# Performance work log

Measured on AMD Instinct MI355X. Metric: run time of the kernel, lower is better.

Reference implementation:

```python
import jax, jax.numpy as jnp
import numpy as np

N_WIRES = 8


def setup_inputs() -> dict:
    key = jax.random.key(0)
    k1, k2, k3 = jax.random.split(key, 3)
    B, S, E = 8, 1024, 64
    x = jax.random.normal(k1, (B, S, E), jnp.float32)
    theta = jax.random.normal(k2, (N_WIRES,), jnp.float32) * 0.1  # trainable RX angles (shared QLayer across heads)
    V_CAT = 16
    combine_w = jax.random.normal(k3, (E, V_CAT), jnp.float32) / jnp.sqrt(jnp.float32(V_CAT))
    combine_b = jnp.zeros((E,), jnp.float32)
    return {"x": x, "theta": theta, "combine_w": combine_w, "combine_b": combine_b}


def _cnot(state, c, t):
    # state: [N] + [2]*N_WIRES ; wire w lives on axis w+1
    ca, ta = c + 1, t + 1
    s0 = jax.lax.index_in_dim(state, 0, axis=ca, keepdims=False)
    s1 = jax.lax.index_in_dim(state, 1, axis=ca, keepdims=False)
    ta2 = ta - 1 if ta > ca else ta  # control axis was removed
    s1 = jnp.flip(s1, axis=ta2)      # flip target bit where control == 1
    return jnp.stack([s0, s1], axis=ca)


def _qlayer(angles, theta):
    # angles: [N, 8]. RX(x) then trainable RX(theta) on same wire == RX(x+theta).
    half = 0.5 * (angles + theta)
    amp0 = jnp.cos(half).astype(jnp.complex64)          # <0|RX|0>
    amp1 = (-1j) * jnp.sin(half).astype(jnp.complex64)  # <1|RX|0>
    N = angles.shape[0]
    # product state over 8 wires -> [N, 256]
    state = jnp.ones((N, 1), jnp.complex64)
    for w in range(N_WIRES):
        per = jnp.stack([amp0[:, w], amp1[:, w]], axis=-1)  # [N, 2]
        state = (state[:, :, None] * per[:, None, :]).reshape(N, -1)
    state = state.reshape((N,) + (2,) * N_WIRES)
    # CNOT chain 0->1, ..., 6->7, then ring closure 7->0
    for w in range(N_WIRES - 1):
        state = _cnot(state, w, w + 1)
    state = _cnot(state, N_WIRES - 1, 0)
    probs = state.real ** 2 + state.imag ** 2
    exps = []
    for w in range(N_WIRES):
        axes = tuple(ax for ax in range(1, N_WIRES + 1) if ax != w + 1)
        marg = probs.sum(axis=axes)  # [N, 2]
        exps.append(marg[:, 0] - marg[:, 1])  # <Z_w>
    return jnp.stack(exps, axis=-1)  # [N, 8]


def reference(x, theta, combine_w, combine_b):
    B, S, E = x.shape
    d_k = E // N_WIRES  # == 8 (encoder needs exactly 8 angles)
    heads = x.reshape(B, S, N_WIRES, d_k).transpose(0, 2, 1, 3)  # [B, H, S, 8]
    meas = _qlayer(heads.reshape(-1, d_k), theta).reshape(B, N_WIRES, S, N_WIRES)
    # torch.chunk(3, -1) on size 8 -> splits of 3, 3, 2
    q, k, v = meas[..., :3], meas[..., 3:6], meas[..., 6:]
    scores = jnp.einsum('bhsd,bhtd->bhst', q, k) / jnp.sqrt(jnp.float32(E))
    attn = jax.nn.softmax(scores, axis=-1)
    out = jnp.einsum('bhst,bhtd->bhsd', attn, v)          # [B, H, S, 2]
    out = out.transpose(0, 2, 1, 3).reshape(B, S, -1)     # [B, S, 16]
    return out @ combine_w.T + combine_b
```

## Files before the change

kernel.cpp:

```cpp
#include <hip/hip_runtime.h>
#include <hip/hip_fp16.h>

#define NB 8
#define NS 1024
#define NH 8

typedef float f2 __attribute__((ext_vector_type(2)));


__global__ __launch_bounds__(256, 2) void attn_fused(
        const float* __restrict__ x, const float* __restrict__ theta,
        float* __restrict__ att) {
    __shared__ float4 kvl[NS];
    __shared__ float  v1l[NS];
    __shared__ float  redS[4][128];
    __shared__ float  redA[4][128];
    __shared__ float  redB[4][128];

    const int tid = threadIdx.x;
    const int bh = blockIdx.x >> 3;
    const int chunk = blockIdx.x & 7;
    const int b = bh >> 3, h = bh & 7;
    const int s0 = chunk * 128;

    float th[8];
#pragma unroll
    for (int j = 0; j < 8; ++j) th[j] = theta[j];

#pragma unroll
    for (int i = 0; i < 4; ++i) {
        int t = tid + i * 256;
        const float4* xp = (const float4*)(x + (((size_t)(b * NS + t)) << 6) + h * 8);
        float4 lo = xp[0], hi = xp[1];
        float c0 = __cosf(lo.x + th[0]);
        float c1 = __cosf(lo.y + th[1]);
        float c2 = __cosf(lo.z + th[2]);
        float c3 = __cosf(lo.w + th[3]);
        float c4 = __cosf(hi.x + th[4]);
        float c5 = __cosf(hi.y + th[5]);
        float c6 = __cosf(hi.z + th[6]);
        float c7 = __cosf(hi.w + th[7]);
        float m3 = ((c0 * c1) * c2) * c3;
        float m4 = m3 * c4;
        float m5 = m4 * c5;
        float m6 = m5 * c6;
        kvl[t] = make_float4(m3, m4, m5, m6);
        v1l[t] = m6 * c7;
    }

    const int ja = tid & 63;
    const int slice = tid >> 6;
    f2 qx, qy, qz;
#pragma unroll
    for (int i = 0; i < 2; ++i) {
        int s = s0 + ja + i * 64;
        const float4* xp = (const float4*)(x + (((size_t)(b * NS + s)) << 6) + h * 8);
        float4 lo = xp[0], hi = xp[1];
        float c0 = __cosf(lo.x + th[0]);
        float c1 = __cosf(lo.y + th[1]);
        float c2 = __cosf(lo.z + th[2]);
        float c3 = __cosf(lo.w + th[3]);
        float c4 = __cosf(hi.x + th[4]);
        float c5 = __cosf(hi.y + th[5]);
        float c6 = __cosf(hi.z + th[6]);
        float c7 = __cosf(hi.w + th[7]);
        float m1 = c0 * c1;
        float m2 = m1 * c2;
        float m0 = ((c1 * c2) * (c3 * c4)) * ((c5 * c6) * c7);
        qx[i] = m0 * 0.125f;
        qy[i] = m1 * 0.125f;
        qz[i] = m2 * 0.125f;
    }
    __syncthreads();

    f2 sum = {0.f, 0.f}, a0 = {0.f, 0.f}, a1 = {0.f, 0.f};
    const int t0 = slice * 256;
#pragma unroll 8
    for (int i = 0; i < 256; ++i) {
        int t = t0 + i;
        float4 kv = kvl[t];
        float v1 = v1l[t];
        f2 d = qx * kv.x + qy * kv.y + qz * kv.z;
        f2 e = {__expf(d.x), __expf(d.y)};
        sum += e;
        a0 += e * kv.w;
        a1 += e * v1;
    }
    redS[slice][ja] = sum.x;  redS[slice][64 + ja] = sum.y;
    redA[slice][ja] = a0.x;   redA[slice][64 + ja] = a0.y;
    redB[slice][ja] = a1.x;   redB[slice][64 + ja] = a1.y;
    __syncthreads();

    if (tid < 128) {
        float S = redS[0][tid] + redS[1][tid] + redS[2][tid] + redS[3][tid];
        float A = redA[0][tid] + redA[1][tid] + redA[2][tid] + redA[3][tid];
        float B = redB[0][tid] + redB[1][tid] + redB[2][tid] + redB[3][tid];
        float inv = 1.0f / S;
        int s = s0 + tid;
        float* o = att + ((size_t)(b * NS + s) * 16) + h * 2;
        o[0] = A * inv;
        o[1] = B * inv;
    }
}

__global__ __launch_bounds__(256, 2) void proj_kernel(
        const float* __restrict__ att, const float* __restrict__ W,
        const float* __restrict__ bias, float* __restrict__ out) {
    __shared__ float WtL[16 * 65];
    __shared__ float biasL[64];
    __shared__ float rowsL[16 * 16];
    const int tid = threadIdx.x;
    const int rbase = blockIdx.x * 16;

    for (int i = tid; i < 1024; i += 256)
        WtL[(i & 15) * 65 + (i >> 4)] = W[i];
    if (tid < 64) biasL[tid] = bias[tid];
    if (tid < 256) rowsL[tid] = att[(size_t)rbase * 16 + tid];
    __syncthreads();

    const int e = tid & 63, rr = tid >> 6;
#pragma unroll
    for (int p = 0; p < 4; ++p) {
        int row = p * 4 + rr;
        float acc = biasL[e];
#pragma unroll
        for (int j = 0; j < 16; ++j)
            acc = fmaf(rowsL[row * 16 + j], WtL[j * 65 + e], acc);
        out[(((size_t)(rbase + row)) << 6) + e] = acc;
    }
}

#define NPAD 1028
#define SPB 32
__global__ __launch_bounds__(256) void fused_kernel(const float* __restrict__ x,
                                                    const float* __restrict__ theta,
                                                    const float* __restrict__ W,
                                                    const float* __restrict__ bias,
                                                    float* __restrict__ out) {
    __shared__ __half2 kvA[NH][NPAD];
    __shared__ __half2 kvB[NH][NPAD];
    __shared__ __half  kvC[NH][NPAD];
    __shared__ float   attl[SPB][17];
    __shared__ float   Wt[16][64];
    __shared__ float   bl[64];

    const int tid = threadIdx.x;
    const int b = blockIdx.x >> 5;
    const int chunk = blockIdx.x & 31;

    float th[8];
#pragma unroll
    for (int j = 0; j < 8; ++j) th[j] = theta[j];

    for (int i = tid; i < 1024; i += 256) Wt[i & 15][i >> 4] = W[i];
    if (tid < 64) bl[tid] = bias[tid];

    for (int i = 0; i < 32; ++i) {
        int r = tid + (i << 8);
        int h = r & 7, t = r >> 3;
        const float4* xp = (const float4*)(x + (((size_t)(b * NS + t)) << 6) + h * 8);
        float4 lo = xp[0], hi = xp[1];
        float c0 = __cosf(lo.x + th[0]);
        float c1 = __cosf(lo.y + th[1]);
        float c2 = __cosf(lo.z + th[2]);
        float c3 = __cosf(lo.w + th[3]);
        float c4 = __cosf(hi.x + th[4]);
        float c5 = __cosf(hi.y + th[5]);
        float c6 = __cosf(hi.z + th[6]);
        float c7 = __cosf(hi.w + th[7]);
        float m3 = ((c0 * c1) * c2) * c3;
        float m4 = m3 * c4;
        float m5 = m4 * c5;
        float m6 = m5 * c6;
        float m7 = m6 * c7;
        kvA[h][t] = __floats2half2_rn(m3, m4);
        kvB[h][t] = __floats2half2_rn(m5, m6);
        kvC[h][t] = __float2half_rn(m7);
    }
    __syncthreads();

    {
        const int h = tid >> 5;
        const int sl = tid & 31;
        const int sg = chunk * SPB + sl;
        const float4* xp = (const float4*)(x + (((size_t)(b * NS + sg)) << 6) + h * 8);
        float4 lo = xp[0], hi = xp[1];
        float c0 = __cosf(lo.x + th[0]);
        float c1 = __cosf(lo.y + th[1]);
        float c2 = __cosf(lo.z + th[2]);
        float c3 = __cosf(lo.w + th[3]);
        float c4 = __cosf(hi.x + th[4]);
        float c5 = __cosf(hi.y + th[5]);
        float c6 = __cosf(hi.z + th[6]);
        float c7 = __cosf(hi.w + th[7]);
        float m1 = c0 * c1;
        float m2 = m1 * c2;
        float m0 = ((c1 * c2) * (c3 * c4)) * ((c5 * c6) * c7);
        float q0 = m0 * 0.125f, q1 = m1 * 0.125f, q2 = m2 * 0.125f;

        float sum = 0.f, a0 = 0.f, a1 = 0.f;
#pragma unroll 4
        for (int t = 0; t < NS; ++t) {
            float2 kk = __half22float2(kvA[h][t]);
            float2 kv = __half22float2(kvB[h][t]);
            float v1 = __half2float(kvC[h][t]);
            float sc = q0 * kk.x + q1 * kk.y + q2 * kv.x;
            float e = __expf(sc);
            sum += e;
            a0 += e * kv.y;
            a1 += e * v1;
        }
        float inv = 1.0f / sum;
        attl[sl][h * 2] = a0 * inv;
        attl[sl][h * 2 + 1] = a1 * inv;
    }
    __syncthreads();

    {
        const int e = tid & 63;
        const int rr = tid >> 6;
#pragma unroll
        for (int i = 0; i < 8; ++i) {
            int sl = rr * 8 + i;
            float acc = bl[e];
#pragma unroll
            for (int j = 0; j < 16; ++j)
                acc += attl[sl][j] * Wt[j][e];
            int sg = chunk * SPB + sl;
            out[(((size_t)(b * NS + sg)) << 6) + e] = acc;
        }
    }
}

extern "C" void kernel_launch(void* const* d_in, const int* in_sizes, int n_in,
                              void* d_out, int out_size, void* d_ws, size_t ws_size,
                              hipStream_t stream) {
    const float* x     = (const float*)d_in[0];
    const float* theta = (const float*)d_in[1];
    const float* W     = (const float*)d_in[2];
    const float* bias  = (const float*)d_in[3];
    float* out = (float*)d_out;

    if (ws_size >= (size_t)NB * NS * 16 * sizeof(float)) {
        float* att = (float*)d_ws;
        attn_fused<<<dim3(NB * NH * 8), dim3(256), 0, stream>>>(x, theta, att);
        proj_kernel<<<dim3(NB * NS / 16), dim3(256), 0, stream>>>(att, W, bias, out);
    } else {
        fused_kernel<<<dim3(NB * (NS / SPB)), dim3(256), 0, stream>>>(x, theta, W, bias, out);
    }
}
```

Before: 81.96 us.

## Register-block four queries per thread and use exp2 in attention loop

```diff
diff --git a/kernel.cpp b/kernel.cpp
--- a/kernel.cpp
+++ b/kernel.cpp
@@ -6,16 +6,22 @@
 #define NH 8
 
 typedef float f2 __attribute__((ext_vector_type(2)));
+
+#if __has_builtin(__builtin_amdgcn_exp2f)
+#define EXP2F(x) __builtin_amdgcn_exp2f(x)
+#else
+#define EXP2F(x) exp2f(x)
+#endif
 
 
 __global__ __launch_bounds__(256, 2) void attn_fused(
         const float* __restrict__ x, const float* __restrict__ theta,
         float* __restrict__ att) {
     __shared__ float4 kvl[NS];
-    __shared__ float  v1l[NS];
-    __shared__ float  redS[4][128];
-    __shared__ float  redA[4][128];
-    __shared__ float  redB[4][128];
+    __shared__ __align__(16) float v1l[NS];
+    __shared__ float redS[8][130];
+    __shared__ float redA[8][130];
+    __shared__ float redB[8][130];
 
     const int tid = threadIdx.x;
     const int bh = blockIdx.x >> 3;
@@ -48,53 +54,87 @@
         v1l[t] = m6 * c7;
     }
 
-    const int ja = tid & 63;
-    const int slice = tid >> 6;
-    f2 qx, qy, qz;
-#pragma unroll
-    for (int i = 0; i < 2; ++i) {
-        int s = s0 + ja + i * 64;
-        const float4* xp = (const float4*)(x + (((size_t)(b * NS + s)) << 6) + h * 8);
-        float4 lo = xp[0], hi = xp[1];
-        float c0 = __cosf(lo.x + th[0]);
-        float c1 = __cosf(lo.y + th[1]);
-        float c2 = __cosf(lo.z + th[2]);
-        float c3 = __cosf(lo.w + th[3]);
-        float c4 = __cosf(hi.x + th[4]);
-        float c5 = __cosf(hi.y + th[5]);
-        float c6 = __cosf(hi.z + th[6]);
-        float c7 = __cosf(hi.w + th[7]);
-        float m1 = c0 * c1;
-        float m2 = m1 * c2;
-        float m0 = ((c1 * c2) * (c3 * c4)) * ((c5 * c6) * c7);
-        qx[i] = m0 * 0.125f;
-        qy[i] = m1 * 0.125f;
-        qz[i] = m2 * 0.125f;
-    }
-    __syncthreads();
-
-    f2 sum = {0.f, 0.f}, a0 = {0.f, 0.f}, a1 = {0.f, 0.f};
-    const int t0 = slice * 256;
-#pragma unroll 8
-    for (int i = 0; i < 256; ++i) {
-        int t = t0 + i;
-        float4 kv = kvl[t];
-        float v1 = v1l[t];
-        f2 d = qx * kv.x + qy * kv.y + qz * kv.z;
-        f2 e = {__expf(d.x), __expf(d.y)};
-        sum += e;
-        a0 += e * kv.w;
-        a1 += e * v1;
-    }
-    redS[slice][ja] = sum.x;  redS[slice][64 + ja] = sum.y;
-    redA[slice][ja] = a0.x;   redA[slice][64 + ja] = a0.y;
-    redB[slice][ja] = a1.x;   redB[slice][64 + ja] = a1.y;
+    const float QSC = 0.125f * 1.44269504088896f;
+    const int sIdx = tid & 31;
+    const int slice = tid >> 5;
+    f2 qx[2], qy[2], qz[2];
+#pragma unroll
+    for (int p = 0; p < 2; ++p)
+#pragma unroll
+        for (int i = 0; i < 2; ++i) {
+            int s = s0 + sIdx + (p * 2 + i) * 32;
+            const float4* xp = (const float4*)(x + (((size_t)(b * NS + s)) << 6) + h * 8);
+            float4 lo = xp[0], hi = xp[1];
+            float c0 = __cosf(lo.x + th[0]);
+            float c1 = __cosf(lo.y + th[1]);
+            float c2 = __cosf(lo.z + th[2]);
+            float c3 = __cosf(lo.w + th[3]);
+            float c4 = __cosf(hi.x + th[4]);
+            float c5 = __cosf(hi.y + th[5]);
+            float c6 = __cosf(hi.z + th[6]);
+            float c7 = __cosf(hi.w + th[7]);
+            float m1 = c0 * c1;
+            float m2 = m1 * c2;
+            float m0 = ((c1 * c2) * (c3 * c4)) * ((c5 * c6) * c7);
+            qx[p][i] = m0 * QSC;
+            qy[p][i] = m1 * QSC;
+            qz[p][i] = m2 * QSC;
+        }
+    __syncthreads();
+
+    f2 sum[2] = {{0.f, 0.f}, {0.f, 0.f}};
+    f2 A0[2]  = {{0.f, 0.f}, {0.f, 0.f}};
+    f2 A1[2]  = {{0.f, 0.f}, {0.f, 0.f}};
+    const int t0 = slice * 128;
+    const float4* v1g4 = (const float4*)v1l;
+#pragma unroll 2
+    for (int g = 0; g < 32; ++g) {
+        float4 v14 = v1g4[(t0 >> 2) + g];
+        float4 kv0 = kvl[t0 + g * 4 + 0];
+        float4 kv1 = kvl[t0 + g * 4 + 1];
+        float4 kv2 = kvl[t0 + g * 4 + 2];
+        float4 kv3 = kvl[t0 + g * 4 + 3];
+        const float vv[4] = {v14.x, v14.y, v14.z, v14.w};
+        const float4 kvs[4] = {kv0, kv1, kv2, kv3};
+#pragma unroll
+        for (int j = 0; j < 4; ++j) {
+            float4 kv = kvs[j];
+            float v1 = vv[j];
+#pragma unroll
+            for (int p = 0; p < 2; ++p) {
+                f2 d = qx[p] * kv.x;
+                d += qy[p] * kv.y;
+                d += qz[p] * kv.z;
+                f2 e = {EXP2F(d.x), EXP2F(d.y)};
+                sum[p] += e;
+                A0[p] += e * kv.w;
+                A1[p] += e * v1;
+            }
+        }
+    }
+
+    redS[slice][sIdx]      = sum[0].x;
+    redS[slice][sIdx + 32] = sum[0].y;
+    redS[slice][sIdx + 64] = sum[1].x;
+    redS[slice][sIdx + 96] = sum[1].y;
+    redA[slice][sIdx]      = A0[0].x;
+    redA[slice][sIdx + 32] = A0[0].y;
+    redA[slice][sIdx + 64] = A0[1].x;
+    redA[slice][sIdx + 96] = A0[1].y;
+    redB[slice][sIdx]      = A1[0].x;
+    redB[slice][sIdx + 32] = A1[0].y;
+    redB[slice][sIdx + 64] = A1[1].x;
+    redB[slice][sIdx + 96] = A1[1].y;
     __syncthreads();
 
     if (tid < 128) {
-        float S = redS[0][tid] + redS[1][tid] + redS[2][tid] + redS[3][tid];
-        float A = redA[0][tid] + redA[1][tid] + redA[2][tid] + redA[3][tid];
-        float B = redB[0][tid] + redB[1][tid] + redB[2][tid] + redB[3][tid];
+        float S = 0.f, A = 0.f, B = 0.f;
+#pragma unroll
+        for (int k = 0; k < 8; ++k) {
+            S += redS[k][tid];
+            A += redA[k][tid];
+            B += redB[k][tid];
+        }
         float inv = 1.0f / S;
         int s = s0 + tid;
         float* o = att + ((size_t)(b * NS + s) * 16) + h * 2;
```

Result: faster. 78.45 us (-4.3%).

## Replace quadratic softmax attention with truncated Taylor moment expansion

Applied to the files above, without the earlier changes.

```diff
diff --git a/kernel.cpp b/kernel.cpp
--- a/kernel.cpp
+++ b/kernel.cpp
@@ -4,33 +4,55 @@
 #define NB 8
 #define NS 1024
 #define NH 8
-
-typedef float f2 __attribute__((ext_vector_type(2)));
-
-
-__global__ __launch_bounds__(256, 2) void attn_fused(
+#define NMONO 56
+
+
+__constant__ int PRED[NMONO] = {
+    0,
+    0, 0, 0,
+    1, 2, 3, 2, 3, 3,
+    4, 5, 6, 7, 8, 9, 7, 8, 9, 9,
+    10,11,12,13,14,15,16,17,18,19,16,17,18,19,19,
+    20,21,22,23,24,25,26,27,28,29,30,31,32,33,34,30,31,32,33,34,34};
+__constant__ int VARI[NMONO] = {
+    0,
+    0, 1, 2,
+    0, 0, 0, 1, 1, 2,
+    0, 0, 0, 0, 0, 0, 1, 1, 1, 2,
+    0, 0, 0, 0, 0, 0, 0, 0, 0, 0, 1, 1, 1, 1, 2,
+    0, 0, 0, 0, 0, 0, 0, 0, 0, 0, 0, 0, 0, 0, 0, 1, 1, 1, 1, 1, 2};
+#define F6 0.166666666666667f
+#define F12 0.0833333333333333f
+#define F24 0.0416666666666667f
+#define F120 0.00833333333333333f
+__constant__ float COEF[NMONO] = {
+    1.f,
+    1.f, 1.f, 1.f,
+    0.5f, 1.f, 1.f, 0.5f, 1.f, 0.5f,
+    F6, 0.5f, 0.5f, 0.5f, 1.f, 0.5f, F6, 0.5f, 0.5f, F6,
+    F24, F6, F6, 0.25f, 0.5f, 0.25f, F6, 0.5f, 0.5f, F6, F24, F6, 0.25f, F6, F24,
+    F120, F24, F24, F12, F6, F12, F12, 0.25f, 0.25f, F12, F24, F6, 0.25f, F6, F24,
+    F120, F24, F12, F12, F24, F120};
+
+__global__ __launch_bounds__(256, 2) void moments_kernel(
         const float* __restrict__ x, const float* __restrict__ theta,
-        float* __restrict__ att) {
-    __shared__ float4 kvl[NS];
-    __shared__ float  v1l[NS];
-    __shared__ float  redS[4][128];
-    __shared__ float  redA[4][128];
-    __shared__ float  redB[4][128];
+        float* __restrict__ part) {
+    __shared__ float4 kv4[256];
+    __shared__ float  v1l[256];
+    __shared__ float  red[3][64][57];
 
     const int tid = threadIdx.x;
-    const int bh = blockIdx.x >> 3;
-    const int chunk = blockIdx.x & 7;
+    const int bh = blockIdx.x >> 2;
+    const int qt = blockIdx.x & 3;
     const int b = bh >> 3, h = bh & 7;
-    const int s0 = chunk * 128;
 
     float th[8];
 #pragma unroll
     for (int j = 0; j < 8; ++j) th[j] = theta[j];
 
-#pragma unroll
-    for (int i = 0; i < 4; ++i) {
-        int t = tid + i * 256;
-        const float4* xp = (const float4*)(x + (((size_t)(b * NS + t)) << 6) + h * 8);
+    {
+        int t = qt * 256 + tid;
+        const float4* xp = (const float4*)(x + ((size_t)(b * NS + t)) * 64 + h * 8);
         float4 lo = xp[0], hi = xp[1];
         float c0 = __cosf(lo.x + th[0]);
         float c1 = __cosf(lo.y + th[1]);
@@ -44,17 +66,80 @@
         float m4 = m3 * c4;
         float m5 = m4 * c5;
         float m6 = m5 * c6;
-        kvl[t] = make_float4(m3, m4, m5, m6);
-        v1l[t] = m6 * c7;
-    }
-
-    const int ja = tid & 63;
-    const int slice = tid >> 6;
-    f2 qx, qy, qz;
-#pragma unroll
-    for (int i = 0; i < 2; ++i) {
-        int s = s0 + ja + i * 64;
-        const float4* xp = (const float4*)(x + (((size_t)(b * NS + s)) << 6) + h * 8);
+        kv4[tid] = make_float4(m3, m4, m5, m6);
+        v1l[tid] = m6 * c7;
+    }
+    __syncthreads();
+
+    const int w = tid >> 6, l = tid & 63;
+    if (w < 3) {
+        float acc[NMONO];
+#pragma unroll
+        for (int i = 0; i < NMONO; ++i) acc[i] = 0.f;
+#pragma unroll
+        for (int j = 0; j < 4; ++j) {
+            float4 kv = kv4[l + 64 * j];
+            float v1 = v1l[l + 64 * j];
+            float wch = (w == 0) ? 1.f : ((w == 1) ? kv.w : v1);
+            float mono[NMONO];
+            mono[0] = wch;
+            acc[0] += wch;
+#pragma unroll
+            for (int i = 1; i < NMONO; ++i) {
+                float var = (VARI[i] == 0) ? kv.x : ((VARI[i] == 1) ? kv.y : kv.z);
+                mono[i] = mono[PRED[i]] * var;
+                acc[i] += mono[i];
+            }
+        }
+#pragma unroll
+        for (int i = 0; i < NMONO; ++i) red[w][l][i] = acc[i];
+    }
+    __syncthreads();
+
+    if (w < 3 && l < NMONO) {
+        float s0 = 0.f, s1 = 0.f, s2 = 0.f, s3 = 0.f;
+#pragma unroll
+        for (int r = 0; r < 16; ++r) {
+            s0 += red[w][4 * r + 0][l];
+            s1 += red[w][4 * r + 1][l];
+            s2 += red[w][4 * r + 2][l];
+            s3 += red[w][4 * r + 3][l];
+        }
+        part[(size_t)blockIdx.x * 168 + w * 56 + l] = (s0 + s1) + (s2 + s3);
+    }
+}
+
+__global__ __launch_bounds__(256, 2) void eval_proj_kernel(
+        const float* __restrict__ x, const float* __restrict__ theta,
+        const float* __restrict__ part, const float* __restrict__ W,
+        const float* __restrict__ bias, float* __restrict__ out) {
+    __shared__ __align__(16) float MhL[8 * 172];
+    __shared__ float WtL[16 * 65];
+    __shared__ float biasL[64];
+    __shared__ float attL[32][17];
+
+    const int tid = threadIdx.x;
+    const int b = blockIdx.x >> 5;
+    const int sc = blockIdx.x & 31;
+    const int s0 = sc * 32;
+
+    for (int e = tid; e < 8 * 168; e += 256) {
+        int h = e / 168, idx = e - h * 168;
+        const float* p = part + ((size_t)((b * 8 + h) * 4)) * 168 + idx;
+        float s = (p[0] + p[168]) + (p[336] + p[504]);
+        MhL[h * 172 + idx] = s * COEF[idx % 56];
+    }
+    for (int i = tid; i < 1024; i += 256) WtL[(i & 15) * 65 + (i >> 4)] = W[i];
+    if (tid < 64) biasL[tid] = bias[tid];
+    __syncthreads();
+
+    {
+        const int h = tid >> 5, sl = tid & 31;
+        const int s = s0 + sl;
+        float th[8];
+#pragma unroll
+        for (int j = 0; j < 8; ++j) th[j] = theta[j];
+        const float4* xp = (const float4*)(x + ((size_t)(b * NS + s)) * 64 + h * 8);
         float4 lo = xp[0], hi = xp[1];
         float c0 = __cosf(lo.x + th[0]);
         float c1 = __cosf(lo.y + th[1]);
@@ -67,66 +152,47 @@
         float m1 = c0 * c1;
         float m2 = m1 * c2;
         float m0 = ((c1 * c2) * (c3 * c4)) * ((c5 * c6) * c7);
-        qx[i] = m0 * 0.125f;
-        qy[i] = m1 * 0.125f;
-        qz[i] = m2 * 0.125f;
-    }
-    __syncthreads();
-
-    f2 sum = {0.f, 0.f}, a0 = {0.f, 0.f}, a1 = {0.f, 0.f};
-    const int t0 = slice * 256;
-#pragma unroll 8
-    for (int i = 0; i < 256; ++i) {
-        int t = t0 + i;
-        float4 kv = kvl[t];
-        float v1 = v1l[t];
-        f2 d = qx * kv.x + qy * kv.y + qz * kv.z;
-        f2 e = {__expf(d.x), __expf(d.y)};
-        sum += e;
-        a0 += e * kv.w;
-        a1 += e * v1;
-    }
-    redS[slice][ja] = sum.x;  redS[slice][64 + ja] = sum.y;
-    redA[slice][ja] = a0.x;   redA[slice][64 + ja] = a0.y;
-    redB[slice][ja] = a1.x;   redB[slice][64 + ja] = a1.y;
-    __syncthreads();
-
-    if (tid < 128) {
-        float S = redS[0][tid] + redS[1][tid] + redS[2][tid] + redS[3][tid];
-        float A = redA[0][tid] + redA[1][tid] + redA[2][tid] + redA[3][tid];
-        float B = redB[0][tid] + redB[1][tid] + redB[2][tid] + redB[3][tid];
-        float inv = 1.0f / S;
-        int s = s0 + tid;
-        float* o = att + ((size_t)(b * NS + s) * 16) + h * 2;
-        o[0] = A * inv;
-        o[1] = B * inv;
-    }
-}
-
-__global__ __launch_bounds__(256, 2) void proj_kernel(
-        const float* __restrict__ att, const float* __restrict__ W,
-        const float* __restrict__ bias, float* __restrict__ out) {
-    __shared__ float WtL[16 * 65];
-    __shared__ float biasL[64];
-    __shared__ float rowsL[16 * 16];
-    const int tid = threadIdx.x;
-    const int rbase = blockIdx.x * 16;
-
-    for (int i = tid; i < 1024; i += 256)
-        WtL[(i & 15) * 65 + (i >> 4)] = W[i];
-    if (tid < 64) biasL[tid] = bias[tid];
-    if (tid < 256) rowsL[tid] = att[(size_t)rbase * 16 + tid];
-    __syncthreads();
-
-    const int e = tid & 63, rr = tid >> 6;
-#pragma unroll
-    for (int p = 0; p < 4; ++p) {
-        int row = p * 4 + rr;
-        float acc = biasL[e];
-#pragma unroll
-        for (int j = 0; j < 16; ++j)
-            acc = fmaf(rowsL[row * 16 + j], WtL[j * 65 + e], acc);
-        out[(((size_t)(rbase + row)) << 6) + e] = acc;
+        float q0 = m0 * 0.125f, q1 = m1 * 0.125f, q2 = m2 * 0.125f;
+
+        float mono[NMONO];
+        mono[0] = 1.f;
+#pragma unroll
+        for (int i = 1; i < NMONO; ++i)
+            mono[i] = mono[PRED[i]] * ((VARI[i] == 0) ? q0 : ((VARI[i] == 1) ? q1 : q2));
+
+        const float4* MS = (const float4*)&MhL[h * 172];
+        const float4* MA = (const float4*)&MhL[h * 172 + 56];
+        const float4* MB = (const float4*)&MhL[h * 172 + 112];
+        float aS = 0.f, aA = 0.f, aB = 0.f;
+#pragma unroll
+        for (int g = 0; g < 14; ++g) {
+            float4 ms = MS[g], ma = MA[g], mb = MB[g];
+            float p0 = mono[g * 4 + 0], p1 = mono[g * 4 + 1];
+            float p2 = mono[g * 4 + 2], p3 = mono[g * 4 + 3];
+            aS = fmaf(p0, ms.x, aS); aS = fmaf(p1, ms.y, aS);
+            aS = fmaf(p2, ms.z, aS); aS = fmaf(p3, ms.w, aS);
+            aA = fmaf(p0, ma.x, aA); aA = fmaf(p1, ma.y, aA);
+            aA = fmaf(p2, ma.z, aA); aA = fmaf(p3, ma.w, aA);
+            aB = fmaf(p0, mb.x, aB); aB = fmaf(p1, mb.y, aB);
+            aB = fmaf(p2, mb.z, aB); aB = fmaf(p3, mb.w, aB);
+        }
+        float inv = 1.0f / aS;
+        attL[sl][2 * h]     = aA * inv;
+        attL[sl][2 * h + 1] = aB * inv;
+    }
+    __syncthreads();
+
+    {
+        const int e = tid & 63, rr = tid >> 6;
+#pragma unroll
+        for (int j = 0; j < 8; ++j) {
+            int row = rr * 8 + j;
+            float acc = biasL[e];
+#pragma unroll
+            for (int jj = 0; jj < 16; ++jj)
+                acc = fmaf(attL[row][jj], WtL[jj * 65 + e], acc);
+            out[((size_t)(b * NS + s0 + row)) * 64 + e] = acc;
+        }
     }
 }
 
@@ -241,10 +307,10 @@
     const float* bias  = (const float*)d_in[3];
     float* out = (float*)d_out;
 
-    if (ws_size >= (size_t)NB * NS * 16 * sizeof(float)) {
-        float* att = (float*)d_ws;
-        attn_fused<<<dim3(NB * NH * 8), dim3(256), 0, stream>>>(x, theta, att);
-        proj_kernel<<<dim3(NB * NS / 16), dim3(256), 0, stream>>>(att, W, bias, out);
+    if (ws_size >= (size_t)256 * 168 * sizeof(float)) {
+        float* part = (float*)d_ws;
+        moments_kernel<<<dim3(256), dim3(256), 0, stream>>>(x, theta, part);
+        eval_proj_kernel<<<dim3(256), dim3(256), 0, stream>>>(x, theta, part, W, bias, out);
     } else {
         fused_kernel<<<dim3(NB * (NS / SPB)), dim3(256), 0, stream>>>(x, theta, W, bias, out);
     }
```

Result: slower. 108.5 us (+32.4%).
